# Kernel optimization log

Measured on AMD Instinct MI355X. Metric: run time of the kernel, lower is better.

## Reference

```python
import jax, jax.numpy as jnp
import numpy as np

N, G, E, B, H = 20000, 32768, 1_000_000, 64, 128

def _lin_w(k, fan_in, fan_out):
    return jax.random.normal(k, (fan_in, fan_out), jnp.float32) / np.sqrt(fan_in)

def setup_inputs() -> dict:
    key = jax.random.key(0)
    ks = jax.random.split(key, 12)
    node_embedding = jax.random.normal(ks[0], (N, H), jnp.float32)
    node_pos = jax.random.uniform(ks[1], (N, 3), jnp.float32)
    grid_pos = jax.random.uniform(ks[2], (G, 3), jnp.float32)
    index_i = jax.random.randint(ks[3], (E,), 0, N, jnp.int32)
    index_j = jax.random.randint(ks[4], (E,), N, N + G, jnp.int32)  # grid ids offset by N
    edge_index = jnp.stack([index_i, index_j], axis=0)
    # orthonormal per-graph frames via QR for realism
    q, _ = jnp.linalg.qr(jax.random.normal(ks[5], (B, 3, 3), jnp.float32))
    batch = jnp.sort(jax.random.randint(ks[6], (N,), 0, B, jnp.int32))
    wk = jax.random.split(ks[7], 6)
    return {
        "node_embedding": node_embedding, "node_pos": node_pos, "grid_pos": grid_pos,
        "edge_index": edge_index, "equi_frames": q, "batch": batch,
        "We1": _lin_w(wk[0], 3, H), "be1": jnp.zeros((H,), jnp.float32),
        "We2": _lin_w(wk[1], H, H), "be2": jnp.zeros((H,), jnp.float32),
        "Wm1": _lin_w(wk[2], 2 * H, H), "bm1": jnp.zeros((H,), jnp.float32),
        "Wm2": _lin_w(wk[3], H, H), "bm2": jnp.zeros((H,), jnp.float32),
        "Wu1": _lin_w(wk[4], H, H), "bu1": jnp.zeros((H,), jnp.float32),
        "Wu2": _lin_w(wk[5], H, H), "bu2": jnp.zeros((H,), jnp.float32),
    }

def _mlp(x, W1, b1, W2, b2):
    return jax.nn.silu(x @ W1 + b1) @ W2 + b2

def reference(node_embedding, node_pos, grid_pos, edge_index, equi_frames, batch,
              We1, be1, We2, be2, Wm1, bm1, Wm2, bm2, Wu1, bu1, Wu2, bu2):
    n_nodes = node_pos.shape[0]
    n_seg = n_nodes + grid_pos.shape[0]
    i, j = edge_index[0], edge_index[1]
    # per-edge gathers
    rel_pos = grid_pos[j - n_nodes] - node_pos[i]          # [E,3]
    frames = equi_frames[batch[i]]                          # [E,3,3]
    local_rel = jnp.einsum('eab,eb->ea', frames, rel_pos)   # frame bmm
    pos_emb = _mlp(local_rel, We1, be1, We2, be2)           # [E,H]
    msg = jnp.concatenate([node_embedding[i], pos_emb], -1) # [E,2H]
    msg = _mlp(msg, Wm1, bm1, Wm2, bm2)                     # [E,H]
    # scatter-mean over destination (grid) index; segments [0,N) receive none
    seg_sum = jax.ops.segment_sum(msg, j, num_segments=n_seg)
    cnt = jax.ops.segment_sum(jnp.ones((j.shape[0],), msg.dtype), j, num_segments=n_seg)
    mean = seg_sum / jnp.maximum(cnt, 1.0)[:, None]         # safe div (torch gives NaN on empty)
    return _mlp(mean, Wu1, bu1, Wu2, bu2)                   # [N+G, H]
```

## Files before the change

### kernel.cpp

```cpp
#include <hip/hip_runtime.h>
#include <hip/hip_fp16.h>

#define HN 128
#define NN 20000
#define GG 32768
#define EE 1000000
#define NSEG (NN + GG)
#define TE 128

typedef _Float16 f16;
typedef __attribute__((ext_vector_type(8))) _Float16 f16x8;
typedef __attribute__((ext_vector_type(4))) float f32x4;

__device__ __forceinline__ int swz_h(int row, int col) {
  int b = (row << 8) + (col << 1);
  b ^= (row & 7) << 4;
  return b >> 1;
}

__device__ __forceinline__ int swz_f(int row, int lcol) {
  int b = (row << 8) + (lcol << 2);
  b ^= (row & 7) << 4;
  return b >> 2;
}

__device__ __forceinline__ float silu_f(float x) {
  float d = 1.0f + __expf(-x);
  return x * __builtin_amdgcn_rcpf(d);
}

__device__ __forceinline__ f32x4 mfma16(f16x8 a, f16x8 b, f32x4 c) {
  return __builtin_amdgcn_mfma_f32_16x16x32_f16(a, b, c, 0, 0, 0);
}

__global__ void prep_kernel(const float* __restrict__ Wm1,
                            const float* __restrict__ Wm2,
                            const float* __restrict__ Wu1,
                            const float* __restrict__ Wu2,
                            const float* __restrict__ We2,
                            const float* __restrict__ be2,
                            const float* __restrict__ bm1,
                            const float* __restrict__ bu1,
                            const float* __restrict__ bu2,
                            const int* __restrict__ eidx,
                            f16* __restrict__ wp, f16* __restrict__ Wcp,
                            float* __restrict__ bvec, float* __restrict__ cvec,
                            int* __restrict__ hist) {
  const int b = blockIdx.x;
  const int tid = threadIdx.x;
  if (b < 320) {
    int p = b * 256 + tid;
    if (p >= 81920) return;
    const float* src; int K, off, q;
    if (p < 32768)      { src = Wm1; K = 256; off = 0;     q = p; }
    else if (p < 49152) { src = Wm2; K = 128; off = 32768; q = p - 32768; }
    else if (p < 65536) { src = Wu1; K = 128; off = 49152; q = p - 49152; }
    else                { src = Wu2; K = 128; off = 65536; q = p - 65536; }
    int KS = K >> 5;
    int t   = q / (KS * 512);
    int rem = q - t * KS * 512;
    int s   = rem >> 9;
    int qq  = rem & 511;
    int lane = qq >> 3, e = qq & 7;
    int k = s * 32 + ((lane >> 4) << 3) + e;
    int n = (t << 4) + (lane & 15);
    wp[off + q] = (f16)src[k * HN + n];
  } else if (b < 385) {
    int bb = b - 320;
    if (bb < 64) {
      int o = bb * 256 + tid;
      int k = o >> 7, n = o & 127;
      float s = 0.0f;
      for (int m = 0; m < 128; m++)
        s += We2[k * HN + m] * Wm1[(128 + m) * HN + n];
      int t = n >> 4, sg = k >> 5;
      int lane = (((k >> 3) & 3) << 4) | (n & 15);
      int e = k & 7;
      Wcp[((size_t)(t * 4 + sg) * 64 + lane) * 8 + e] = (f16)s;
    } else {
      if (tid < 128) {
        float s = bm1[tid];
        for (int m = 0; m < 128; m++) s += be2[m] * Wm1[(128 + m) * HN + tid];
        bvec[tid] = s;
      } else {
        int n = tid - 128;
        float s = bu2[n];
        for (int m = 0; m < 128; m++) s += silu_f(bu1[m]) * Wu2[m * HN + n];
        cvec[n] = s;
      }
    }
  } else {
    int e = (b - 385) * 256 + tid;
    if (e < EE) atomicAdd(&hist[eidx[EE + e] - NN], 1);
  }
}

__global__ __launch_bounds__(1024) void scan_kernel(const int* __restrict__ hist,
                                                    int* __restrict__ cursor) {
  __shared__ int sbuf[1024];
  int tid = threadIdx.x;
  int base = tid * 32;
  int v[32];
  int s = 0;
#pragma unroll
  for (int k = 0; k < 32; k++) { int t = hist[base + k]; v[k] = s; s += t; }
  int tot = s;
  sbuf[tid] = s;
  __syncthreads();
  for (int off = 1; off < 1024; off <<= 1) {
    int x = (tid >= off) ? sbuf[tid - off] : 0;
    __syncthreads();
    sbuf[tid] += x;
    __syncthreads();
  }
  int excl = sbuf[tid] - tot;
#pragma unroll
  for (int k = 0; k < 32; k++) cursor[base + k] = excl + v[k];
}

__global__ void reorder_kernel(const int* __restrict__ eidx,
                               int* __restrict__ cursor, int2* __restrict__ sij) {
  int e = blockIdx.x * 256 + threadIdx.x;
  if (e < EE) {
    int j = eidx[EE + e];
    int p = atomicAdd(&cursor[j - NN], 1);
    sij[p] = make_int2(eidx[e], j);
  }
}

__global__ __launch_bounds__(256, 2) void ynode_kernel(
    const float* __restrict__ emb, const f16* __restrict__ Wm1p,
    const float* __restrict__ bvec, f16* __restrict__ Ynode) {
  __shared__ __align__(16) f16 A1[TE * HN];
  const int tid = threadIdx.x;
  const int rbase = blockIdx.x * TE;

  for (int idx = tid; idx < TE * HN; idx += 256) {
    int e = idx >> 7, h = idx & (HN - 1);
    int row = rbase + e;
    float v = (row < NN) ? emb[(size_t)row * HN + h] : 0.0f;
    A1[swz_h(e, h)] = (f16)v;
  }
  __syncthreads();

  const int lane = tid & 63;
  const int w = tid >> 6;
  const int lr_ = lane & 15;
  const int hi = lane >> 4;
  const int r0w = w * 32;

  f16x8 a[2][4];
#pragma unroll
  for (int mt = 0; mt < 2; mt++)
#pragma unroll
    for (int s = 0; s < 4; s++)
      a[mt][s] = *(const f16x8*)(A1 + swz_h(r0w + mt * 16 + lr_, s * 32 + hi * 8));

  f32x4 acc[2][8];
#pragma unroll
  for (int t = 0; t < 8; t++) {
    float bv = bvec[t * 16 + lr_];
    acc[0][t] = (f32x4){bv, bv, bv, bv};
    acc[1][t] = (f32x4){bv, bv, bv, bv};
  }
#pragma unroll
  for (int t = 0; t < 8; t++)
#pragma unroll
    for (int s = 0; s < 4; s++) {
      f16x8 b = *(const f16x8*)(Wm1p + (size_t)((t * 8 + s) * 64 + lane) * 8);
      acc[0][t] = mfma16(a[0][s], b, acc[0][t]);
      acc[1][t] = mfma16(a[1][s], b, acc[1][t]);
    }
#pragma unroll
  for (int mt = 0; mt < 2; mt++)
#pragma unroll
    for (int t = 0; t < 8; t++)
#pragma unroll
      for (int r = 0; r < 4; r++) {
        int row = rbase + r0w + mt * 16 + hi * 4 + r;
        if (row < NN)
          Ynode[(size_t)row * HN + t * 16 + lr_] = (f16)acc[mt][t][r];
      }
}

__global__ __launch_bounds__(256, 4) void edge_kernel(
    const f16* __restrict__ Ynode, const float* __restrict__ npos,
    const float* __restrict__ gpos, const float* __restrict__ frames,
    const int* __restrict__ batch, const int2* __restrict__ sij,
    const float* __restrict__ We1, const float* __restrict__ be1,
    const f16* __restrict__ Wcp, float* __restrict__ out) {
  __shared__ __align__(16) float M[TE * 64];
  __shared__ float sW[4 * HN];
  __shared__ float sLR[TE * 3];
  __shared__ int sI[TE];
  __shared__ int sJ[TE];

  const int tid = threadIdx.x;
  const int ebase = blockIdx.x * TE;

  for (int k = tid; k < 4 * HN; k += 256)
    sW[k] = (k < 3 * HN) ? We1[k] : be1[k - 3 * HN];

  if (tid < TE) {
    int p = ebase + tid;
    bool valid = p < EE;
    int2 ij = sij[valid ? p : 0];
    int i = ij.x;
    int g = ij.y - NN;
    float r0 = gpos[g * 3 + 0] - npos[i * 3 + 0];
    float r1 = gpos[g * 3 + 1] - npos[i * 3 + 1];
    float r2 = gpos[g * 3 + 2] - npos[i * 3 + 2];
    const float* F = frames + batch[i] * 9;
    sLR[tid * 3 + 0] = F[0] * r0 + F[1] * r1 + F[2] * r2;
    sLR[tid * 3 + 1] = F[3] * r0 + F[4] * r1 + F[5] * r2;
    sLR[tid * 3 + 2] = F[6] * r0 + F[7] * r1 + F[8] * r2;
    sI[tid] = i;
    sJ[tid] = valid ? ij.y : -1;
  }
  __syncthreads();

  const int lane = tid & 63;
  const int w = tid >> 6;
  const int lr_ = lane & 15;
  const int hi = lane >> 4;
  const int r0w = w * 32;

  const int row0 = r0w + lr_, row1 = r0w + 16 + lr_;
  const float l00 = sLR[row0 * 3], l01 = sLR[row0 * 3 + 1], l02 = sLR[row0 * 3 + 2];
  const float l10 = sLR[row1 * 3], l11 = sLR[row1 * 3 + 1], l12 = sLR[row1 * 3 + 2];
  f16x8 afr[2][4];
#pragma unroll
  for (int s = 0; s < 4; s++) {
    f16x8 a0, a1;
#pragma unroll
    for (int e = 0; e < 8; e++) {
      int k = s * 32 + hi * 8 + e;
      float w0 = sW[k], w1 = sW[HN + k], w2 = sW[2 * HN + k], wb = sW[3 * HN + k];
      a0[e] = (f16)silu_f(fmaf(l02, w2, fmaf(l01, w1, fmaf(l00, w0, wb))));
      a1[e] = (f16)silu_f(fmaf(l12, w2, fmaf(l11, w1, fmaf(l10, w0, wb))));
    }
    afr[0][s] = a0; afr[1][s] = a1;
  }

  f32x4 acc[2][8];
#pragma unroll
  for (int mt = 0; mt < 2; mt++)
#pragma unroll
    for (int t = 0; t < 8; t++) acc[mt][t] = (f32x4){0.f, 0.f, 0.f, 0.f};
#pragma unroll
  for (int t = 0; t < 8; t++)
#pragma unroll
    for (int s = 0; s < 4; s++) {
      f16x8 b = *(const f16x8*)(Wcp + (size_t)((t * 4 + s) * 64 + lane) * 8);
      acc[0][t] = mfma16(afr[0][s], b, acc[0][t]);
      acc[1][t] = mfma16(afr[1][s], b, acc[1][t]);
    }

  #pragma unroll
  for (int mt = 0; mt < 2; mt++)
#pragma unroll
    for (int r = 0; r < 4; r++) {
      int row = r0w + mt * 16 + hi * 4 + r;
      const f16* yp = Ynode + (size_t)sI[row] * HN + lr_;
#pragma unroll
      for (int t = 0; t < 8; t++)
        acc[mt][t][r] = silu_f(acc[mt][t][r] + (float)yp[t * 16]);
    }

#pragma unroll
  for (int half = 0; half < 2; half++) {
    if (half) __syncthreads();
#pragma unroll
    for (int mt = 0; mt < 2; mt++)
#pragma unroll
      for (int tq = 0; tq < 4; tq++)
#pragma unroll
        for (int r = 0; r < 4; r++)
          M[swz_f(r0w + mt * 16 + hi * 4 + r, tq * 16 + lr_)] =
              acc[mt][half * 4 + tq][r];
    __syncthreads();
    const int colg = half * 64 + lane;
    float run = 0.0f;
    int jcur = -2;
#pragma unroll
    for (int k = 0; k < 32; k++) {
      int row = r0w + k;
      int jr = sJ[row];
      float v = M[swz_f(row, lane)];
      if (jr != jcur) {
        if (jcur >= 0) atomicAdd(&out[(size_t)jcur * HN + colg], run);
        run = 0.0f;
        jcur = jr;
      }
      if (jr >= 0) run += v;
    }
    if (jcur >= 0) atomicAdd(&out[(size_t)jcur * HN + colg], run);
  }
}

__global__ __launch_bounds__(256, 2) void finalize_kernel(
    float* __restrict__ out, const int* __restrict__ hist,
    const f16* __restrict__ Wm2p, const float* __restrict__ bm2,
    const f16* __restrict__ Wu1p, const float* __restrict__ bu1,
    const f16* __restrict__ Wu2p, const float* __restrict__ bu2,
    const float* __restrict__ cvec) {
  __shared__ __align__(16) f16 A1[TE * HN];
  __shared__ float sb[TE];
  const int tid = threadIdx.x;
  const int rbase = NN + blockIdx.x * TE;

  for (int idx = tid; idx < TE * HN; idx += 256) {
    int e = idx >> 7, h = idx & (HN - 1);
    int c = hist[rbase + e - NN];
    float v = out[(size_t)(rbase + e) * HN + h] / fmaxf((float)c, 1.0f);
    A1[swz_h(e, h)] = (f16)v;
    if (h == 0) sb[e] = (c > 0) ? 1.0f : 0.0f;
  }
  __syncthreads();

  const int lane = tid & 63;
  const int w = tid >> 6;
  const int lr_ = lane & 15;
  const int hi = lane >> 4;
  const int r0w = w * 32;

  f32x4 acc[2][8];

  {
    f16x8 a[2][4];
#pragma unroll
    for (int mt = 0; mt < 2; mt++)
#pragma unroll
      for (int s = 0; s < 4; s++)
        a[mt][s] = *(const f16x8*)(A1 + swz_h(r0w + mt * 16 + lr_, s * 32 + hi * 8));
#pragma unroll
    for (int mt = 0; mt < 2; mt++)
#pragma unroll
      for (int t = 0; t < 8; t++) {
        float bb = bm2[t * 16 + lr_];
        f32x4 c;
#pragma unroll
        for (int r = 0; r < 4; r++) c[r] = bb * sb[r0w + mt * 16 + hi * 4 + r];
        acc[mt][t] = c;
      }
#pragma unroll
    for (int t = 0; t < 8; t++)
#pragma unroll
      for (int s = 0; s < 4; s++) {
        f16x8 b = *(const f16x8*)(Wm2p + (size_t)((t * 4 + s) * 64 + lane) * 8);
        acc[0][t] = mfma16(a[0][s], b, acc[0][t]);
        acc[1][t] = mfma16(a[1][s], b, acc[1][t]);
      }
  }
  __syncthreads();
#pragma unroll
  for (int mt = 0; mt < 2; mt++)
#pragma unroll
    for (int t = 0; t < 8; t++)
#pragma unroll
      for (int r = 0; r < 4; r++)
        A1[swz_h(r0w + mt * 16 + hi * 4 + r, t * 16 + lr_)] = (f16)acc[mt][t][r];
  __syncthreads();

  {
    f16x8 a[2][4];
#pragma unroll
    for (int mt = 0; mt < 2; mt++)
#pragma unroll
      for (int s = 0; s < 4; s++)
        a[mt][s] = *(const f16x8*)(A1 + swz_h(r0w + mt * 16 + lr_, s * 32 + hi * 8));
#pragma unroll
    for (int t = 0; t < 8; t++) {
      float bv = bu1[t * 16 + lr_];
      acc[0][t] = (f32x4){bv, bv, bv, bv};
      acc[1][t] = (f32x4){bv, bv, bv, bv};
    }
#pragma unroll
    for (int t = 0; t < 8; t++)
#pragma unroll
      for (int s = 0; s < 4; s++) {
        f16x8 b = *(const f16x8*)(Wu1p + (size_t)((t * 4 + s) * 64 + lane) * 8);
        acc[0][t] = mfma16(a[0][s], b, acc[0][t]);
        acc[1][t] = mfma16(a[1][s], b, acc[1][t]);
      }
  }
  __syncthreads();
#pragma unroll
  for (int mt = 0; mt < 2; mt++)
#pragma unroll
    for (int t = 0; t < 8; t++)
#pragma unroll
      for (int r = 0; r < 4; r++)
        A1[swz_h(r0w + mt * 16 + hi * 4 + r, t * 16 + lr_)] = (f16)silu_f(acc[mt][t][r]);
  __syncthreads();

  {
    f16x8 a[2][4];
#pragma unroll
    for (int mt = 0; mt < 2; mt++)
#pragma unroll
      for (int s = 0; s < 4; s++)
        a[mt][s] = *(const f16x8*)(A1 + swz_h(r0w + mt * 16 + lr_, s * 32 + hi * 8));
#pragma unroll
    for (int t = 0; t < 8; t++) {
      float bv = bu2[t * 16 + lr_];
      acc[0][t] = (f32x4){bv, bv, bv, bv};
      acc[1][t] = (f32x4){bv, bv, bv, bv};
    }
#pragma unroll
    for (int t = 0; t < 8; t++)
#pragma unroll
      for (int s = 0; s < 4; s++) {
        f16x8 b = *(const f16x8*)(Wu2p + (size_t)((t * 4 + s) * 64 + lane) * 8);
        acc[0][t] = mfma16(a[0][s], b, acc[0][t]);
        acc[1][t] = mfma16(a[1][s], b, acc[1][t]);
      }
  }
#pragma unroll
  for (int mt = 0; mt < 2; mt++)
#pragma unroll
    for (int t = 0; t < 8; t++)
#pragma unroll
      for (int r = 0; r < 4; r++) {
        int row = rbase + r0w + mt * 16 + hi * 4 + r;
        out[(size_t)row * HN + t * 16 + lr_] = acc[mt][t][r];
      }

  for (int i = blockIdx.x * 256 + tid; i < NN * HN / 4; i += 256 * 256) {
    float4 v = reinterpret_cast<const float4*>(cvec)[i & 31];
    reinterpret_cast<float4*>(out)[i] = v;
  }
}

extern "C" void kernel_launch(void* const* d_in, const int* in_sizes, int n_in,
                              void* d_out, int out_size, void* d_ws, size_t ws_size,
                              hipStream_t stream) {
  const float* emb    = (const float*)d_in[0];
  const float* npos   = (const float*)d_in[1];
  const float* gpos   = (const float*)d_in[2];
  const int*   eidx   = (const int*)d_in[3];
  const float* frames = (const float*)d_in[4];
  const int*   batch  = (const int*)d_in[5];
  const float* We1 = (const float*)d_in[6];
  const float* be1 = (const float*)d_in[7];
  const float* We2 = (const float*)d_in[8];
  const float* be2 = (const float*)d_in[9];
  const float* Wm1 = (const float*)d_in[10];
  const float* bm1 = (const float*)d_in[11];
  const float* Wm2 = (const float*)d_in[12];
  const float* bm2 = (const float*)d_in[13];
  const float* Wu1 = (const float*)d_in[14];
  const float* bu1 = (const float*)d_in[15];
  const float* Wu2 = (const float*)d_in[16];
  const float* bu2 = (const float*)d_in[17];

  float* out  = (float*)d_out;
  char* ws    = (char*)d_ws;
  int* hist   = (int*)ws;
  int* cursor = (int*)(ws + 131072);
  f16* wp     = (f16*)(ws + 262144);
  f16* Wm1p   = wp;
  f16* Wm2p   = wp + 32768;
  f16* Wu1p   = wp + 49152;
  f16* Wu2p   = wp + 65536;
  f16* Wcp    = (f16*)(ws + 425984);
  float* bvec = (float*)(ws + 458752);
  float* cvec = (float*)(ws + 459264);
  int2* sij   = (int2*)(ws + 524288);
  f16* Ynode  = (f16*)(ws + 8524288);

  hipMemsetAsync(out + (size_t)NN * HN, 0, (size_t)GG * HN * sizeof(float), stream);
  hipMemsetAsync(hist, 0, (size_t)GG * sizeof(int), stream);

  int hb = (EE + 255) / 256;
  prep_kernel<<<385 + hb, 256, 0, stream>>>(
      Wm1, Wm2, Wu1, Wu2, We2, be2, bm1, bu1, bu2, eidx,
      wp, Wcp, bvec, cvec, hist);

  scan_kernel<<<1, 1024, 0, stream>>>(hist, cursor);
  reorder_kernel<<<hb, 256, 0, stream>>>(eidx, cursor, sij);
  ynode_kernel<<<(NN + TE - 1) / TE, 256, 0, stream>>>(emb, Wm1p, bvec, Ynode);

  int eblocks = (EE + TE - 1) / TE;
  edge_kernel<<<eblocks, 256, 0, stream>>>(
      Ynode, npos, gpos, frames, batch, sij, We1, be1, Wcp, out);

  finalize_kernel<<<GG / TE, 256, 0, stream>>>(out, hist, Wm2p, bm2,
                                               Wu1p, bu1, Wu2p, bu2, cvec);
}
```

Measured before the change: 409.2 us.

## Fold output memset and reorder into existing kernels, split edge epilogue into halves

The memset of the grid output region moves into extra blocks of prep_kernel, and the edge reorder scatter is merged with the ynode GEMM into a single launch. Both changes remove kernel launches and let independent work run concurrently. The edge kernel now computes the 128 output columns in two halves of 64, which lowers peak accumulator registers and may raise occupancy. The cost is extra block-index branching and the loss of interleaving between the two halves' MFMA work.

```diff
diff --git a/kernel.cpp b/kernel.cpp
--- a/kernel.cpp
+++ b/kernel.cpp
@@ -7,6 +7,8 @@
 #define EE 1000000
 #define NSEG (NN + GG)
 #define TE 128
+#define HB 3907
+#define YB 157
 
 typedef _Float16 f16;
 typedef __attribute__((ext_vector_type(8))) _Float16 f16x8;
@@ -45,7 +47,7 @@
                             const int* __restrict__ eidx,
                             f16* __restrict__ wp, f16* __restrict__ Wcp,
                             float* __restrict__ bvec, float* __restrict__ cvec,
-                            int* __restrict__ hist) {
+                            int* __restrict__ hist, float* __restrict__ out) {
   const int b = blockIdx.x;
   const int tid = threadIdx.x;
   if (b < 320) {
@@ -89,9 +91,13 @@
         cvec[n] = s;
       }
     }
-  } else {
+  } else if (b < 385 + HB) {
     int e = (b - 385) * 256 + tid;
     if (e < EE) atomicAdd(&hist[eidx[EE + e] - NN], 1);
+  } else {
+    int i = (b - 385 - HB) * 256 + tid;
+    float4 z = {0.f, 0.f, 0.f, 0.f};
+    reinterpret_cast<float4*>(out)[NN * HN / 4 + i] = z;
   }
 }
 
@@ -118,23 +124,25 @@
   for (int k = 0; k < 32; k++) cursor[base + k] = excl + v[k];
 }
 
-__global__ void reorder_kernel(const int* __restrict__ eidx,
-                               int* __restrict__ cursor, int2* __restrict__ sij) {
-  int e = blockIdx.x * 256 + threadIdx.x;
-  if (e < EE) {
-    int j = eidx[EE + e];
-    int p = atomicAdd(&cursor[j - NN], 1);
-    sij[p] = make_int2(eidx[e], j);
-  }
-}
-
-__global__ __launch_bounds__(256, 2) void ynode_kernel(
+__global__ __launch_bounds__(256, 2) void sort_ynode_kernel(
+    const int* __restrict__ eidx, int* __restrict__ cursor,
+    int2* __restrict__ sij,
     const float* __restrict__ emb, const f16* __restrict__ Wm1p,
     const float* __restrict__ bvec, f16* __restrict__ Ynode) {
   __shared__ __align__(16) f16 A1[TE * HN];
   const int tid = threadIdx.x;
+
+  if (blockIdx.x >= YB) {
+    int e = (blockIdx.x - YB) * 256 + tid;
+    if (e < EE) {
+      int j = eidx[EE + e];
+      int p = atomicAdd(&cursor[j - NN], 1);
+      sij[p] = make_int2(eidx[e], j);
+    }
+    return;
+  }
+
   const int rbase = blockIdx.x * TE;
-
   for (int idx = tid; idx < TE * HN; idx += 256) {
     int e = idx >> 7, h = idx & (HN - 1);
     int row = rbase + e;
@@ -242,44 +250,45 @@
     afr[0][s] = a0; afr[1][s] = a1;
   }
 
-  f32x4 acc[2][8];
-#pragma unroll
-  for (int mt = 0; mt < 2; mt++)
-#pragma unroll
-    for (int t = 0; t < 8; t++) acc[mt][t] = (f32x4){0.f, 0.f, 0.f, 0.f};
-#pragma unroll
-  for (int t = 0; t < 8; t++)
-#pragma unroll
-    for (int s = 0; s < 4; s++) {
-      f16x8 b = *(const f16x8*)(Wcp + (size_t)((t * 4 + s) * 64 + lane) * 8);
-      acc[0][t] = mfma16(afr[0][s], b, acc[0][t]);
-      acc[1][t] = mfma16(afr[1][s], b, acc[1][t]);
-    }
-
-  #pragma unroll
-  for (int mt = 0; mt < 2; mt++)
-#pragma unroll
-    for (int r = 0; r < 4; r++) {
-      int row = r0w + mt * 16 + hi * 4 + r;
-      const f16* yp = Ynode + (size_t)sI[row] * HN + lr_;
-#pragma unroll
-      for (int t = 0; t < 8; t++)
-        acc[mt][t][r] = silu_f(acc[mt][t][r] + (float)yp[t * 16]);
-    }
-
-#pragma unroll
-  for (int half = 0; half < 2; half++) {
-    if (half) __syncthreads();
+#pragma unroll
+  for (int hf = 0; hf < 2; hf++) {
+    f32x4 acc[2][4];
+#pragma unroll
+    for (int mt = 0; mt < 2; mt++)
+#pragma unroll
+      for (int tq = 0; tq < 4; tq++) acc[mt][tq] = (f32x4){0.f, 0.f, 0.f, 0.f};
+#pragma unroll
+    for (int tq = 0; tq < 4; tq++)
+#pragma unroll
+      for (int s = 0; s < 4; s++) {
+        f16x8 b = *(const f16x8*)(Wcp +
+            (size_t)(((hf * 4 + tq) * 4 + s) * 64 + lane) * 8);
+        acc[0][tq] = mfma16(afr[0][s], b, acc[0][tq]);
+        acc[1][tq] = mfma16(afr[1][s], b, acc[1][tq]);
+      }
+
+#pragma unroll
+    for (int mt = 0; mt < 2; mt++)
+#pragma unroll
+      for (int r = 0; r < 4; r++) {
+        int row = r0w + mt * 16 + hi * 4 + r;
+        const f16* yp = Ynode + (size_t)sI[row] * HN + hf * 64 + lr_;
+#pragma unroll
+        for (int tq = 0; tq < 4; tq++)
+          acc[mt][tq][r] = silu_f(acc[mt][tq][r] + (float)yp[tq * 16]);
+      }
+
+    if (hf) __syncthreads();
 #pragma unroll
     for (int mt = 0; mt < 2; mt++)
 #pragma unroll
       for (int tq = 0; tq < 4; tq++)
 #pragma unroll
         for (int r = 0; r < 4; r++)
-          M[swz_f(r0w + mt * 16 + hi * 4 + r, tq * 16 + lr_)] =
-              acc[mt][half * 4 + tq][r];
+          M[swz_f(r0w + mt * 16 + hi * 4 + r, tq * 16 + lr_)] = acc[mt][tq][r];
     __syncthreads();
-    const int colg = half * 64 + lane;
+
+    const int colg = hf * 64 + lane;
     float run = 0.0f;
     int jcur = -2;
 #pragma unroll
@@ -469,17 +478,16 @@
   int2* sij   = (int2*)(ws + 524288);
   f16* Ynode  = (f16*)(ws + 8524288);
 
-  hipMemsetAsync(out + (size_t)NN * HN, 0, (size_t)GG * HN * sizeof(float), stream);
   hipMemsetAsync(hist, 0, (size_t)GG * sizeof(int), stream);
 
-  int hb = (EE + 255) / 256;
-  prep_kernel<<<385 + hb, 256, 0, stream>>>(
+  prep_kernel<<<385 + HB + 4096, 256, 0, stream>>>(
       Wm1, Wm2, Wu1, Wu2, We2, be2, bm1, bu1, bu2, eidx,
-      wp, Wcp, bvec, cvec, hist);
+      wp, Wcp, bvec, cvec, hist, out);
 
   scan_kernel<<<1, 1024, 0, stream>>>(hist, cursor);
-  reorder_kernel<<<hb, 256, 0, stream>>>(eidx, cursor, sij);
-  ynode_kernel<<<(NN + TE - 1) / TE, 256, 0, stream>>>(emb, Wm1p, bvec, Ynode);
+
+  sort_ynode_kernel<<<YB + HB, 256, 0, stream>>>(
+      eidx, cursor, sij, emb, Wm1p, bvec, Ynode);
 
   int eblocks = (EE + TE - 1) / TE;
   edge_kernel<<<eblocks, 256, 0, stream>>>(
```

After: 436.7 us. 6.7% more time.
